# Kernel tuning notes

Measured on AMD Instinct MI355X. Metric: run time of the kernel, lower is better.

The kernel has to match this reference:

```python
import jax, jax.numpy as jnp
import numpy as np

B, S, D, H, SEP = 4, 2048, 768, 8, 102
Dh = D // H


def layer_norm(x, g, b, eps=1e-5):
    m = jnp.mean(x, axis=-1, keepdims=True)
    v = jnp.var(x, axis=-1, keepdims=True)
    return (x - m) / jnp.sqrt(v + eps) * g + b


def setup_inputs() -> dict:
    key = jax.random.key(0)
    ks = jax.random.split(key, 16)
    hidden_states = jax.random.normal(ks[0], (B, S, D), dtype=jnp.float32)
    # input_ids: random vocab ids avoiding SEP, with two SEP tokens planted per row
    rng = np.random.default_rng(0)
    ids = rng.integers(103, 30000, size=(B, S))
    for b in range(B):
        ids[b, S // 3 + 7 * b] = SEP
        ids[b, 2 * S // 3 + 11 * b] = SEP
    input_ids = jnp.asarray(ids, dtype=jnp.int64)
    attention_mask = jnp.ones((B, S), dtype=jnp.int32)
    sc = 0.02
    p = {}
    p['Wq'] = jax.random.normal(ks[1], (D, D), jnp.float32) * sc
    p['bq'] = jnp.zeros((D,), jnp.float32)
    p['Wk'] = jax.random.normal(ks[2], (D, D), jnp.float32) * sc
    p['bk'] = jnp.zeros((D,), jnp.float32)
    p['Wv'] = jax.random.normal(ks[3], (D, D), jnp.float32) * sc
    p['bv'] = jnp.zeros((D,), jnp.float32)
    p['Wo'] = jax.random.normal(ks[4], (D, D), jnp.float32) * sc
    p['bo'] = jnp.zeros((D,), jnp.float32)
    p['ln1_g'] = jnp.ones((D,), jnp.float32)
    p['ln1_b'] = jnp.zeros((D,), jnp.float32)
    p['W1'] = jax.random.normal(ks[5], (D, D), jnp.float32) * sc  # d_ff = d_model
    p['b1'] = jnp.zeros((D,), jnp.float32)
    p['W2'] = jax.random.normal(ks[6], (D, D), jnp.float32) * sc
    p['b2'] = jnp.zeros((D,), jnp.float32)
    p['ln2_g'] = jnp.ones((D,), jnp.float32)
    p['ln2_b'] = jnp.zeros((D,), jnp.float32)
    p['dn_g'] = jnp.ones((D,), jnp.float32)
    p['dn_b'] = jnp.zeros((D,), jnp.float32)
    return dict(hidden_states=hidden_states, input_ids=input_ids,
                attention_mask=attention_mask, **p)


def reference(hidden_states, input_ids, attention_mask,
              Wq, bq, Wk, bk, Wv, bv, Wo, bo, ln1_g, ln1_b,
              W1, b1, W2, b2, ln2_g, ln2_b, dn_g, dn_b):
    x = hidden_states
    # --- SEP-based ragged segment discovery (vectorized over batch) ---
    sep = input_ids == SEP                       # [B,S]
    idx = jnp.arange(S)
    big = S
    first = jnp.min(jnp.where(sep, idx, big), axis=-1)                       # [B]
    second = jnp.min(jnp.where(sep & (idx[None, :] > first[:, None]), idx, big), axis=-1)
    has2 = second < big                          # >= 2 SEP tokens present
    mid = S // 2
    src_end = jnp.where(has2, first, mid)
    hyp_start = jnp.where(has2, first + 1, mid)
    hyp_end = jnp.where(has2, second, S - 1)
    src_mask = (idx[None, :] >= 1) & (idx[None, :] < src_end[:, None])       # keys [B,S]
    hyp_mask = (idx[None, :] >= hyp_start[:, None]) & (idx[None, :] < hyp_end[:, None])
    valid = jnp.any(src_mask, -1) & jnp.any(hyp_mask, -1)                    # [B]

    # --- cross-attention: queries = hyp tokens, keys/values = src tokens ---
    q = (x @ Wq + bq).reshape(B, S, H, Dh)
    k = (x @ Wk + bk).reshape(B, S, H, Dh)
    v = (x @ Wv + bv).reshape(B, S, H, Dh)
    scores = jnp.einsum('bqhd,bkhd->bhqk', q, k) / jnp.sqrt(jnp.float32(Dh))
    scores = jnp.where(src_mask[:, None, None, :], scores, jnp.float32(-1e9))
    attn = jax.nn.softmax(scores, axis=-1)
    ctx = jnp.einsum('bhqk,bkhd->bqhd', attn, v).reshape(B, S, D)
    mha = ctx @ Wo + bo
    x1 = layer_norm(x + mha, ln1_g, ln1_b)
    ffn = jax.nn.gelu(x1 @ W1 + b1) @ W2 + b2
    x2 = layer_norm(x1 + ffn, ln2_g, ln2_b)      # updated_hyp

    # --- diff + LayerNorm, scatter back into hyp segment only ---
    diff = layer_norm(x2 - x, dn_g, dn_b)
    upd = hyp_mask & valid[:, None]
    return jnp.where(upd[..., None], x + diff, x)
```

## Files before the change

kernel.cpp:

```cpp
#include <hip/hip_runtime.h>
#include <math.h>

#define BB 4
#define SS 2048
#define DD 768
#define HH 8
#define DHD 96
#define SEP_ID 102
#define CHUNK 256
#define NCH_MAX 3
#define QT64 11
#define SLOTB 12800

typedef __attribute__((ext_vector_type(8))) short bf16x8;
typedef __attribute__((ext_vector_type(4))) float f32x4;

static __device__ __forceinline__ float gelu_tanh(float x) {
  float x3 = x * x * x;
  float t = tanhf(0.7978845608028654f * (x + 0.044715f * x3));
  return 0.5f * x * (1.0f + t);
}

static __device__ __forceinline__ unsigned short f2bf(float f) {
  unsigned int u = __float_as_uint(f);
  u = (u + 0x7FFF + ((u >> 16) & 1)) >> 16;
  return (unsigned short)u;
}

static __device__ __forceinline__ float bf2f(unsigned short u) {
  return __uint_as_float(((unsigned int)u) << 16);
}

#define MFMA16(A, B, C) __builtin_amdgcn_mfma_f32_16x16x32_bf16(A, B, C, 0, 0, 0)

static __device__ __forceinline__ void gl16(const void* g, void* l) {
  __builtin_amdgcn_global_load_lds(
      (__attribute__((address_space(1))) unsigned int*)g,
      (__attribute__((address_space(3))) unsigned int*)l, 16, 0, 0);
}

__global__ __launch_bounds__(256) void prep(
    const int* __restrict__ ids, int* __restrict__ seg,
    const float* __restrict__ x, unsigned short* __restrict__ xbf, int n4,
    const float* __restrict__ W0, const float* __restrict__ W1,
    const float* __restrict__ W2, const float* __restrict__ W3,
    const float* __restrict__ W4, const float* __restrict__ W5,
    unsigned short* __restrict__ Wt) {
  __shared__ char smem[64 * 65 * 4];
  int bx = blockIdx.x;
  if (bx < 4) {
    int* s1 = (int*)smem;
    int* s2 = s1 + 256;
    int b = bx;
    const int* row = ids + (size_t)b * SS;
    int m1 = SS, m2 = SS;
    for (int i = threadIdx.x; i < SS; i += 256) {
      if (row[i] == SEP_ID) {
        if (i < m1) { m2 = m1; m1 = i; }
        else if (i < m2) { m2 = i; }
      }
    }
    s1[threadIdx.x] = m1; s2[threadIdx.x] = m2;
    __syncthreads();
    for (int off = 128; off > 0; off >>= 1) {
      if (threadIdx.x < off) {
        int a1 = s1[threadIdx.x], a2 = s2[threadIdx.x];
        int b1 = s1[threadIdx.x + off], b2 = s2[threadIdx.x + off];
        s1[threadIdx.x] = min(a1, b1);
        s2[threadIdx.x] = min(max(a1, b1), min(a2, b2));
      }
      __syncthreads();
    }
    if (threadIdx.x == 0) {
      int first = s1[0], second = s2[0];
      bool has2 = (second < SS);
      int mid = SS / 2;
      int src_end = has2 ? first : mid;
      int hyp_lo = has2 ? (first + 1) : mid;
      int hyp_hi = has2 ? second : (SS - 1);
      int valid = ((src_end - 1) > 0 && (hyp_hi - hyp_lo) > 0) ? 1 : 0;
      if (!valid) { src_end = 1; hyp_lo = 0; hyp_hi = 0; }
      seg[b * 4 + 0] = src_end;
      seg[b * 4 + 1] = hyp_lo;
      seg[b * 4 + 2] = hyp_hi;
      seg[b * 4 + 3] = valid;
    }
  } else if (bx < 1540) {
    int i = (bx - 4) * 256 + threadIdx.x;
    int stride = 1536 * 256;
    const float4* xi = (const float4*)x;
    for (; i < n4; i += stride) {
      float4 v = xi[i];
      ushort4 r;
      r.x = f2bf(v.x); r.y = f2bf(v.y); r.z = f2bf(v.z); r.w = f2bf(v.w);
      *(ushort4*)(xbf + (size_t)i * 4) = r;
    }
  } else {
    float (*t)[65] = (float(*)[65])smem;
    int idx = bx - 1540;
    int z = idx / 144, rem = idx - z * 144;
    const float* W = (z == 0) ? W0 : (z == 1) ? W1 : (z == 2) ? W2
                    : (z == 3) ? W3 : (z == 4) ? W4 : W5;
    unsigned short* O = Wt + (size_t)z * DD * DD;
    int k0 = (rem / 12) * 64, n0 = (rem % 12) * 64;
    for (int i = threadIdx.x; i < 4096; i += 256) {
      int kk = i >> 6, nn = i & 63;
      t[kk][nn] = W[(size_t)(k0 + kk) * DD + n0 + nn];
    }
    __syncthreads();
    for (int i = threadIdx.x; i < 4096; i += 256) {
      int nn = i >> 6, kk = i & 63;
      O[(size_t)(n0 + nn) * DD + k0 + kk] = f2bf(t[kk][nn]);
    }
  }
}

__device__ __forceinline__ void gemm_core(
    const unsigned short* __restrict__ A, const unsigned short* __restrict__ Wt,
    const float* __restrict__ bias, unsigned short* __restrict__ C,
    int b, int row0, int hi, int col0, int which, float rs,
    unsigned short (*Al)[64 * 64], unsigned short (*Bl)[128 * 64]) {
  int tid = threadIdx.x, w = tid >> 6, lane = tid & 63;
  int llo = lane & 15, lhi = lane >> 4;
  int wrg = w >> 1, wcg = w & 1;

  const unsigned short* Ab = A + (size_t)b * SS * DD;

  f32x4 acc[2][4];
#pragma unroll
  for (int i = 0; i < 2; ++i)
#pragma unroll
    for (int j = 0; j < 4; ++j) acc[i][j] = (f32x4){0.f, 0.f, 0.f, 0.f};

  auto STAGE = [&](int t, int buf) {
    int kk = t * 64;
#pragma unroll
    for (int j = 0; j < 2; ++j) {
      int s = j * 256 + tid;
      int row = s >> 3, c = s & 7;
      int gr = min(row0 + row, hi - 1);
      gl16(Ab + (size_t)gr * DD + kk + ((c ^ (row & 7)) * 8),
           &Al[buf][(size_t)(j * 256 + w * 64) * 8]);
    }
#pragma unroll
    for (int j = 0; j < 4; ++j) {
      int s = j * 256 + tid;
      int row = s >> 3, c = s & 7;
      gl16(Wt + (size_t)(col0 + row) * DD + kk + ((c ^ (row & 7)) * 8),
           &Bl[buf][(size_t)(j * 256 + w * 64) * 8]);
    }
  };

  STAGE(0, 0);
  __syncthreads();
  for (int t = 0; t < DD / 64; ++t) {
    int cur = t & 1;
    if (t + 1 < DD / 64) STAGE(t + 1, cur ^ 1);
#pragma unroll
    for (int ksub = 0; ksub < 2; ++ksub) {
      bf16x8 af[2], bfr[4];
#pragma unroll
      for (int mi = 0; mi < 2; ++mi) {
        int lr = wrg * 32 + mi * 16 + llo;
        int slot = lr * 8 + ((ksub * 4 + lhi) ^ (lr & 7));
        af[mi] = *(const bf16x8*)&Al[cur][(size_t)slot * 8];
      }
#pragma unroll
      for (int ni = 0; ni < 4; ++ni) {
        int lr = wcg * 64 + ni * 16 + llo;
        int slot = lr * 8 + ((ksub * 4 + lhi) ^ (lr & 7));
        bfr[ni] = *(const bf16x8*)&Bl[cur][(size_t)slot * 8];
      }
#pragma unroll
      for (int mi = 0; mi < 2; ++mi)
#pragma unroll
        for (int ni = 0; ni < 4; ++ni)
          acc[mi][ni] = MFMA16(af[mi], bfr[ni], acc[mi][ni]);
    }
    __syncthreads();
  }

  float osc = (which == 0) ? rs : 1.f;
#pragma unroll
  for (int mi = 0; mi < 2; ++mi)
#pragma unroll
    for (int ni = 0; ni < 4; ++ni) {
      int col = col0 + wcg * 64 + ni * 16 + llo;
      float bsv = bias[col];
      int rowb = row0 + wrg * 32 + mi * 16 + lhi * 4;
#pragma unroll
      for (int r = 0; r < 4; ++r) {
        int row = rowb + r;
        if (which == 2) {
          float v = acc[mi][ni][r] + bsv;
          C[((size_t)b * DD + col) * SS + row] =
              (row < hi) ? f2bf(v) : (unsigned short)0;
        } else if (row < hi) {
          float v = (acc[mi][ni][r] + bsv) * osc;
          if (which == 4) v = gelu_tanh(v);
          C[((size_t)(b * SS + row)) * DD + col] = f2bf(v);
        }
      }
    }
}

__global__ __launch_bounds__(256) void gemm_qkv(
    const unsigned short* __restrict__ A, const unsigned short* __restrict__ Wt3,
    const float* __restrict__ bq, const float* __restrict__ bk, const float* __restrict__ bv,
    unsigned short* __restrict__ Qo, unsigned short* __restrict__ Ko,
    unsigned short* __restrict__ Vto, const int* __restrict__ seg, float rs) {
  __shared__ unsigned short Al[2][64 * 64];
  __shared__ unsigned short Bl[2][128 * 64];
  int b = blockIdx.z;
  int which = blockIdx.x / 6;
  int col0 = (blockIdx.x % 6) * 128;
  int lo = (which == 0) ? seg[b * 4 + 1] : 1;
  int hi = (which == 0) ? seg[b * 4 + 2] : seg[b * 4 + 0];
  int row0 = lo + (int)blockIdx.y * 64;
  if (row0 >= hi && !(which == 2 && row0 < hi + 64)) return;
  const unsigned short* Wt = Wt3 + (size_t)which * DD * DD;
  const float* bias = (which == 0) ? bq : (which == 1) ? bk : bv;
  unsigned short* C = (which == 0) ? Qo : (which == 1) ? Ko : Vto;
  gemm_core(A, Wt, bias, C, b, row0, hi, col0, which, rs, Al, Bl);
}

__global__ __launch_bounds__(256) void gemm_mfma(
    const unsigned short* __restrict__ A, const unsigned short* __restrict__ Wt,
    const float* __restrict__ bias, unsigned short* __restrict__ C,
    const int* __restrict__ seg, int gelu) {
  __shared__ unsigned short Al[2][64 * 64];
  __shared__ unsigned short Bl[2][128 * 64];
  int b = blockIdx.z;
  int lo = seg[b * 4 + 1], hi = seg[b * 4 + 2];
  int row0 = lo + (int)blockIdx.y * 64;
  if (row0 >= hi) return;
  gemm_core(A, Wt, bias, C, b, row0, hi, (int)blockIdx.x * 128,
            gelu ? 4 : 3, 1.f, Al, Bl);
}

__global__ __launch_bounds__(256) void attn_split(
    const unsigned short* __restrict__ Q, const unsigned short* __restrict__ K,
    const unsigned short* __restrict__ Vt, char* __restrict__ part,
    const int* __restrict__ seg) {
  int bh = blockIdx.z;
  int b = bh >> 3, h = bh & 7;
  int src_hi = seg[b * 4 + 0];
  int hyp_lo = seg[b * 4 + 1], hyp_hi = seg[b * 4 + 2];
  int q0b = hyp_lo + (int)blockIdx.x * 64;
  if (q0b >= hyp_hi) return;
  int ks = 1 + (int)blockIdx.y * CHUNK;
  if (ks >= src_hi) return;
  int ke = min(ks + CHUNK, src_hi);

  __shared__ unsigned short kls[64 * 128];
  __shared__ unsigned short vls[96 * 64];
  __shared__ unsigned short plds[4][1024];

  int tid = threadIdx.x;
  int w = tid >> 6, lane = tid & 63;
  int llo = lane & 15, lhi = lane >> 4;

  int qrow = min(q0b + w * 16 + llo, hyp_hi - 1);
  const unsigned short* qbase = Q + ((size_t)(b * SS + qrow)) * DD + h * DHD;
  bf16x8 qf[3];
#pragma unroll
  for (int df = 0; df < 3; ++df)
    qf[df] = *(const bf16x8*)(qbase + df * 32 + lhi * 8);

  const unsigned short* Kb = K + (size_t)b * SS * DD + h * DHD;
  const unsigned short* Vb = Vt + ((size_t)b * DD + h * DHD) * SS;

  f32x4 acc[6];
#pragma unroll
  for (int dt = 0; dt < 6; ++dt) acc[dt] = (f32x4){0.f, 0.f, 0.f, 0.f};
  float m_r[4] = {-1e30f, -1e30f, -1e30f, -1e30f};
  float l_r[4] = {0.f, 0.f, 0.f, 0.f};

  for (int k0 = ks; k0 < ke; k0 += 64) {
    __syncthreads();
#pragma unroll
    for (int p = 0; p < 3; ++p) {
      int idx = tid + p * 256;
      int row = idx / 12, slot = idx - row * 12;
      int krow = min(k0 + row, ke - 1);
      bf16x8 v = *(const bf16x8*)(Kb + (size_t)krow * DD + slot * 8);
      *(bf16x8*)&kls[row * 128 + ((slot ^ (row & 7)) << 3)] = v;
    }
#pragma unroll
    for (int p = 0; p < 3; ++p) {
      int idx = tid + p * 256;
      int row = idx >> 3, slot = idx & 7;
      bf16x8 v = *(const bf16x8*)(Vb + (size_t)row * SS + k0 + slot * 8);
      *(bf16x8*)&vls[row * 64 + ((slot ^ (row & 7)) << 3)] = v;
    }
    __syncthreads();
    f32x4 s[4];
#pragma unroll
    for (int t = 0; t < 4; ++t) {
      f32x4 st = (f32x4){0.f, 0.f, 0.f, 0.f};
      int row = t * 16 + llo;
#pragma unroll
      for (int df = 0; df < 3; ++df) {
        int slot = df * 4 + lhi;
        bf16x8 kf = *(const bf16x8*)&kls[row * 128 + ((slot ^ (row & 7)) << 3)];
        st = MFMA16(qf[df], kf, st);
      }
      s[t] = st;
    }
    float mx[4] = {-1e30f, -1e30f, -1e30f, -1e30f};
#pragma unroll
    for (int t = 0; t < 4; ++t) {
      bool kv = (k0 + t * 16 + llo) < ke;
#pragma unroll
      for (int r = 0; r < 4; ++r) {
        float sv = kv ? s[t][r] : -1e30f;
        s[t][r] = sv;
        mx[r] = fmaxf(mx[r], sv);
      }
    }
#pragma unroll
    for (int st = 1; st < 16; st <<= 1)
#pragma unroll
      for (int r = 0; r < 4; ++r) mx[r] = fmaxf(mx[r], __shfl_xor(mx[r], st));

    float p[4][4];
#pragma unroll
    for (int r = 0; r < 4; ++r) {
      float mn = fmaxf(m_r[r], mx[r]);
      float sc = __expf(m_r[r] - mn);
      m_r[r] = mn;
      l_r[r] *= sc;
#pragma unroll
      for (int dt = 0; dt < 6; ++dt) acc[dt][r] *= sc;
      float ps = 0.f;
#pragma unroll
      for (int t = 0; t < 4; ++t) {
        float pv = (s[t][r] > -1e29f) ? __expf(s[t][r] - mn) : 0.f;
        p[t][r] = pv;
        ps += pv;
      }
#pragma unroll
      for (int st = 1; st < 16; st <<= 1) ps += __shfl_xor(ps, st);
      l_r[r] += ps;
    }
#pragma unroll
    for (int t = 0; t < 4; ++t)
#pragma unroll
      for (int r = 0; r < 4; ++r) {
        int qq = lhi * 4 + r, kk = t * 16 + llo;
        plds[w][qq * 64 + (kk ^ ((qq & 7) << 3))] = f2bf(p[t][r]);
      }
    bf16x8 pa[2];
#pragma unroll
    for (int kh = 0; kh < 2; ++kh) {
      int idx = llo * 64 + ((lhi * 8 + kh * 32) ^ ((llo & 7) << 3));
      pa[kh] = *(const bf16x8*)&plds[w][idx];
    }
#pragma unroll
    for (int dt = 0; dt < 6; ++dt) {
      int row = dt * 16 + llo;
#pragma unroll
      for (int kh = 0; kh < 2; ++kh) {
        int slot = kh * 4 + lhi;
        bf16x8 vf = *(const bf16x8*)&vls[row * 64 + ((slot ^ (row & 7)) << 3)];
        acc[dt] = MFMA16(pa[kh], vf, acc[dt]);
      }
    }
  }
  char* slot = part + (((size_t)bh * QT64 + blockIdx.x) * NCH_MAX + blockIdx.y) * SLOTB;
  unsigned short* pacc = (unsigned short*)slot;
  float* pml = (float*)(slot + 12288);
#pragma unroll
  for (int r = 0; r < 4; ++r) {
    int qq = w * 16 + lhi * 4 + r;
#pragma unroll
    for (int dt = 0; dt < 6; ++dt)
      pacc[qq * 96 + dt * 16 + llo] = f2bf(acc[dt][r]);
    if (llo == 0) { pml[qq] = m_r[r]; pml[64 + qq] = l_r[r]; }
  }
}

__global__ __launch_bounds__(128) void attn_reduce(
    const char* __restrict__ part, unsigned short* __restrict__ ctx,
    const int* __restrict__ seg) {
  int bh = blockIdx.y;
  int b = bh >> 3, h = bh & 7;
  int src_hi = seg[b * 4 + 0];
  int hyp_lo = seg[b * 4 + 1], hyp_hi = seg[b * 4 + 2];
  int q0 = hyp_lo + (int)blockIdx.x * 16;
  if (q0 >= hyp_hi) return;
  int nch = (src_hi - 1 + CHUNK - 1) / CHUNK;
  if (nch > NCH_MAX) nch = NCH_MAX;
  int sub = blockIdx.x & 3;

  __shared__ float ml[NCH_MAX][32];
  __shared__ float Mg[16], invL[16], sc[NCH_MAX][16];
  int tid = threadIdx.x;
  const char* base = part + ((size_t)bh * QT64 + (blockIdx.x >> 2)) * NCH_MAX * SLOTB;
  for (int i = tid; i < 32 * nch; i += 128) {
    int c = i >> 5, j = i & 31;
    const float* pml = (const float*)(base + c * SLOTB + 12288);
    ml[c][j] = (j < 16) ? pml[sub * 16 + j] : pml[64 + sub * 16 + (j - 16)];
  }
  __syncthreads();
  if (tid < 16) {
    float mg = -1e30f;
    for (int c = 0; c < nch; ++c) mg = fmaxf(mg, ml[c][tid]);
    float lg = 0.f;
    for (int c = 0; c < nch; ++c) lg += ml[c][16 + tid] * __expf(ml[c][tid] - mg);
    Mg[tid] = mg;
    invL[tid] = 1.f / lg;
  }
  __syncthreads();
  for (int i = tid; i < 16 * nch; i += 128) {
    int c = i >> 4, q = i & 15;
    sc[c][q] = __expf(ml[c][q] - Mg[q]);
  }
  __syncthreads();
  for (int i = tid; i < 1536; i += 128) {
    int q = i / 96, d = i - q * 96;
    float v = 0.f;
    for (int c = 0; c < nch; ++c)
      v += bf2f(((const unsigned short*)(base + c * SLOTB))[(sub * 16 + q) * 96 + d]) * sc[c][q];
    int qq = q0 + q;
    if (qq < hyp_hi)
      ctx[((size_t)(b * SS + qq)) * DD + h * DHD + d] = f2bf(v * invL[q]);
  }
}

__device__ __forceinline__ float block_sum(float v, float* sbuf) {
#pragma unroll
  for (int off = 32; off > 0; off >>= 1) v += __shfl_xor(v, off);
  int lane = threadIdx.x & 63, w = threadIdx.x >> 6;
  __syncthreads();
  if (lane == 0) sbuf[w] = v;
  __syncthreads();
  return sbuf[0] + sbuf[1] + sbuf[2] + sbuf[3];
}

__global__ __launch_bounds__(256) void ln_residual(
    const float* __restrict__ X, const unsigned short* __restrict__ Yin,
    const float* __restrict__ g, const float* __restrict__ bta,
    float* __restrict__ Out, unsigned short* __restrict__ OutBf,
    const int* __restrict__ seg) {
  int b = blockIdx.y;
  int row = seg[b * 4 + 1] + (int)blockIdx.x;
  if (row >= seg[b * 4 + 2]) return;
  __shared__ float sbuf[4];
  size_t base = ((size_t)(b * SS + row)) * DD;
  int tid = threadIdx.x;
  float v[3];
  float sum = 0.f;
#pragma unroll
  for (int r = 0; r < 3; ++r) {
    int i = tid + r * 256;
    v[r] = X[base + i] + bf2f(Yin[base + i]);
    sum += v[r];
  }
  float mean = block_sum(sum, sbuf) * (1.f / DD);
  float vs = 0.f;
#pragma unroll
  for (int r = 0; r < 3; ++r) { float d = v[r] - mean; vs += d * d; }
  float var = block_sum(vs, sbuf) * (1.f / DD);
  float inv = rsqrtf(var + 1e-5f);
#pragma unroll
  for (int r = 0; r < 3; ++r) {
    int i = tid + r * 256;
    float o = (v[r] - mean) * inv * g[i] + bta[i];
    Out[base + i] = o;
    OutBf[base + i] = f2bf(o);
  }
}

__global__ __launch_bounds__(256) void ln2_diff_scatter(
    const float* __restrict__ X, const float* __restrict__ X1,
    const unsigned short* __restrict__ T2,
    const float* __restrict__ g2, const float* __restrict__ b2,
    const float* __restrict__ gd, const float* __restrict__ bd,
    float* __restrict__ Out, const int* __restrict__ seg) {
  int b = blockIdx.y, row = blockIdx.x;
  size_t base = ((size_t)(b * SS + row)) * DD;
  int tid = threadIdx.x;
  if (row < seg[b * 4 + 1] || row >= seg[b * 4 + 2]) {
#pragma unroll
    for (int r = 0; r < 3; ++r) {
      int i = tid + r * 256;
      Out[base + i] = X[base + i];
    }
    return;
  }
  __shared__ float sbuf[4];
  float y[3], xv[3];
  float sum = 0.f;
#pragma unroll
  for (int r = 0; r < 3; ++r) {
    int i = tid + r * 256;
    y[r] = X1[base + i] + bf2f(T2[base + i]);
    xv[r] = X[base + i];
    sum += y[r];
  }
  float mean = block_sum(sum, sbuf) * (1.f / DD);
  float vs = 0.f;
#pragma unroll
  for (int r = 0; r < 3; ++r) { float d = y[r] - mean; vs += d * d; }
  float var = block_sum(vs, sbuf) * (1.f / DD);
  float inv = rsqrtf(var + 1e-5f);
  float z[3];
  float sum2 = 0.f;
#pragma unroll
  for (int r = 0; r < 3; ++r) {
    int i = tid + r * 256;
    float x2 = (y[r] - mean) * inv * g2[i] + b2[i];
    z[r] = x2 - xv[r];
    sum2 += z[r];
  }
  float mean2 = block_sum(sum2, sbuf) * (1.f / DD);
  float vs2 = 0.f;
#pragma unroll
  for (int r = 0; r < 3; ++r) { float d = z[r] - mean2; vs2 += d * d; }
  float var2 = block_sum(vs2, sbuf) * (1.f / DD);
  float inv2 = rsqrtf(var2 + 1e-5f);
#pragma unroll
  for (int r = 0; r < 3; ++r) {
    int i = tid + r * 256;
    Out[base + i] = xv[r] + (z[r] - mean2) * inv2 * gd[i] + bd[i];
  }
}

extern "C" void kernel_launch(void* const* d_in, const int* in_sizes, int n_in,
                              void* d_out, int out_size, void* d_ws, size_t ws_size,
                              hipStream_t stream) {
  const float* x = (const float*)d_in[0];
  const int* ids = (const int*)d_in[1];
  const float* Wq = (const float*)d_in[3];
  const float* bq = (const float*)d_in[4];
  const float* Wk = (const float*)d_in[5];
  const float* bk = (const float*)d_in[6];
  const float* Wv = (const float*)d_in[7];
  const float* bv = (const float*)d_in[8];
  const float* Wo = (const float*)d_in[9];
  const float* bo = (const float*)d_in[10];
  const float* ln1g = (const float*)d_in[11];
  const float* ln1b = (const float*)d_in[12];
  const float* W1 = (const float*)d_in[13];
  const float* b1 = (const float*)d_in[14];
  const float* W2 = (const float*)d_in[15];
  const float* b2 = (const float*)d_in[16];
  const float* ln2g = (const float*)d_in[17];
  const float* ln2b = (const float*)d_in[18];
  const float* dng = (const float*)d_in[19];
  const float* dnb = (const float*)d_in[20];
  float* out = (float*)d_out;

  char* ws = (char*)d_ws;
  int* seg = (int*)ws;
  size_t NBH = (size_t)BB * SS * DD * 2;
  char* Ap = ws + 256;
  char* Bp = Ap + NBH;
  char* Cp = Bp + NBH;
  char* Dp = Cp + NBH;
  char* Fp = Dp + NBH + 8192;
  char* Gp = Fp + (size_t)BB * SS * DD * 4;

  unsigned short* x_bf = (unsigned short*)Ap;
  unsigned short* ctx_bf = (unsigned short*)Ap;
  unsigned short* h1_bf = (unsigned short*)Ap;
  unsigned short* q_bf = (unsigned short*)Bp;
  unsigned short* mha_bf = (unsigned short*)Bp;
  unsigned short* k_bf = (unsigned short*)Cp;
  unsigned short* t2_bf = (unsigned short*)Cp;
  unsigned short* vt_bf = (unsigned short*)Dp;
  unsigned short* x1_bf = (unsigned short*)Dp;
  char* part = Fp;
  float* x1f = (float*)Fp;
  unsigned short* wt = (unsigned short*)Gp;
  const size_t WSZ = (size_t)DD * DD;

  const float rs = 0.1020620726159658f;

  prep<<<2404, 256, 0, stream>>>(ids, seg, x, x_bf, BB * SS * DD / 4,
                                 Wq, Wk, Wv, Wo, W1, W2, wt);

  gemm_qkv<<<dim3(18, 12, BB), 256, 0, stream>>>(
      x_bf, wt, bq, bk, bv, q_bf, k_bf, vt_bf, seg, rs);

  attn_split<<<dim3(QT64, NCH_MAX, 32), 256, 0, stream>>>(q_bf, k_bf, vt_bf, part, seg);
  attn_reduce<<<dim3(44, 32), 128, 0, stream>>>(part, ctx_bf, seg);

  gemm_mfma<<<dim3(6, 11, BB), 256, 0, stream>>>(ctx_bf, wt + 3 * WSZ, bo, mha_bf, seg, 0);
  ln_residual<<<dim3(704, BB), 256, 0, stream>>>(x, mha_bf, ln1g, ln1b, x1f, x1_bf, seg);
  gemm_mfma<<<dim3(6, 11, BB), 256, 0, stream>>>(x1_bf, wt + 4 * WSZ, b1, h1_bf, seg, 1);
  gemm_mfma<<<dim3(6, 11, BB), 256, 0, stream>>>(h1_bf, wt + 5 * WSZ, b2, t2_bf, seg, 0);
  ln2_diff_scatter<<<dim3(SS, BB), 256, 0, stream>>>(x, x1f, t2_bf, ln2g, ln2b, dng, dnb, out, seg);
}
```

Measured before the change: 166.3 us.

## Halve GEMM K-tile to 32, drop swizzle, and remove fp32 x1 buffer

The shared GEMM core now stages a K-depth of 32 instead of 64 per iteration, with one A load and two B loads per thread and no XOR swizzle on LDS addresses. This halves LDS use per block, which may raise occupancy, but it doubles the number of barrier-synchronised iterations and may bring back LDS bank conflicts. Separately, the first LayerNorm no longer writes an fp32 copy of x1; the final LN kernel reads the bf16 copy instead. That saves a global write and read but lowers the precision of the residual path.

```diff
diff --git a/kernel.cpp b/kernel.cpp
--- a/kernel.cpp
+++ b/kernel.cpp
@@ -119,7 +119,7 @@
     const unsigned short* __restrict__ A, const unsigned short* __restrict__ Wt,
     const float* __restrict__ bias, unsigned short* __restrict__ C,
     int b, int row0, int hi, int col0, int which, float rs,
-    unsigned short (*Al)[64 * 64], unsigned short (*Bl)[128 * 64]) {
+    unsigned short (*Al)[64 * 32], unsigned short (*Bl)[128 * 32]) {
   int tid = threadIdx.x, w = tid >> 6, lane = tid & 63;
   int llo = lane & 15, lhi = lane >> 4;
   int wrg = w >> 1, wcg = w & 1;
@@ -132,51 +132,43 @@
 #pragma unroll
     for (int j = 0; j < 4; ++j) acc[i][j] = (f32x4){0.f, 0.f, 0.f, 0.f};
 
+  int arow = tid >> 2, ac = tid & 3;
+  int agr = min(row0 + arow, hi - 1);
+  const unsigned short* asrc = Ab + (size_t)agr * DD + ac * 8;
+
   auto STAGE = [&](int t, int buf) {
-    int kk = t * 64;
+    int kk = t * 32;
+    gl16(asrc + kk, &Al[buf][(size_t)(w * 64) * 8]);
 #pragma unroll
     for (int j = 0; j < 2; ++j) {
       int s = j * 256 + tid;
-      int row = s >> 3, c = s & 7;
-      int gr = min(row0 + row, hi - 1);
-      gl16(Ab + (size_t)gr * DD + kk + ((c ^ (row & 7)) * 8),
-           &Al[buf][(size_t)(j * 256 + w * 64) * 8]);
-    }
-#pragma unroll
-    for (int j = 0; j < 4; ++j) {
-      int s = j * 256 + tid;
-      int row = s >> 3, c = s & 7;
-      gl16(Wt + (size_t)(col0 + row) * DD + kk + ((c ^ (row & 7)) * 8),
+      int row = s >> 2, c = s & 3;
+      gl16(Wt + (size_t)(col0 + row) * DD + kk + c * 8,
            &Bl[buf][(size_t)(j * 256 + w * 64) * 8]);
     }
   };
 
   STAGE(0, 0);
   __syncthreads();
-  for (int t = 0; t < DD / 64; ++t) {
+  for (int t = 0; t < DD / 32; ++t) {
     int cur = t & 1;
-    if (t + 1 < DD / 64) STAGE(t + 1, cur ^ 1);
-#pragma unroll
-    for (int ksub = 0; ksub < 2; ++ksub) {
-      bf16x8 af[2], bfr[4];
-#pragma unroll
-      for (int mi = 0; mi < 2; ++mi) {
-        int lr = wrg * 32 + mi * 16 + llo;
-        int slot = lr * 8 + ((ksub * 4 + lhi) ^ (lr & 7));
-        af[mi] = *(const bf16x8*)&Al[cur][(size_t)slot * 8];
-      }
-#pragma unroll
-      for (int ni = 0; ni < 4; ++ni) {
-        int lr = wcg * 64 + ni * 16 + llo;
-        int slot = lr * 8 + ((ksub * 4 + lhi) ^ (lr & 7));
-        bfr[ni] = *(const bf16x8*)&Bl[cur][(size_t)slot * 8];
-      }
-#pragma unroll
-      for (int mi = 0; mi < 2; ++mi)
-#pragma unroll
-        for (int ni = 0; ni < 4; ++ni)
-          acc[mi][ni] = MFMA16(af[mi], bfr[ni], acc[mi][ni]);
-    }
+    if (t + 1 < DD / 32) STAGE(t + 1, cur ^ 1);
+    bf16x8 af[2], bfr[4];
+#pragma unroll
+    for (int mi = 0; mi < 2; ++mi) {
+      int lr = wrg * 32 + mi * 16 + llo;
+      af[mi] = *(const bf16x8*)&Al[cur][lr * 32 + lhi * 8];
+    }
+#pragma unroll
+    for (int ni = 0; ni < 4; ++ni) {
+      int lr = wcg * 64 + ni * 16 + llo;
+      bfr[ni] = *(const bf16x8*)&Bl[cur][lr * 32 + lhi * 8];
+    }
+#pragma unroll
+    for (int mi = 0; mi < 2; ++mi)
+#pragma unroll
+      for (int ni = 0; ni < 4; ++ni)
+        acc[mi][ni] = MFMA16(af[mi], bfr[ni], acc[mi][ni]);
     __syncthreads();
   }
 
@@ -209,8 +201,8 @@
     const float* __restrict__ bq, const float* __restrict__ bk, const float* __restrict__ bv,
     unsigned short* __restrict__ Qo, unsigned short* __restrict__ Ko,
     unsigned short* __restrict__ Vto, const int* __restrict__ seg, float rs) {
-  __shared__ unsigned short Al[2][64 * 64];
-  __shared__ unsigned short Bl[2][128 * 64];
+  __shared__ unsigned short Al[2][64 * 32];
+  __shared__ unsigned short Bl[2][128 * 32];
   int b = blockIdx.z;
   int which = blockIdx.x / 6;
   int col0 = (blockIdx.x % 6) * 128;
@@ -228,8 +220,8 @@
     const unsigned short* __restrict__ A, const unsigned short* __restrict__ Wt,
     const float* __restrict__ bias, unsigned short* __restrict__ C,
     const int* __restrict__ seg, int gelu) {
-  __shared__ unsigned short Al[2][64 * 64];
-  __shared__ unsigned short Bl[2][128 * 64];
+  __shared__ unsigned short Al[2][64 * 32];
+  __shared__ unsigned short Bl[2][128 * 32];
   int b = blockIdx.z;
   int lo = seg[b * 4 + 1], hi = seg[b * 4 + 2];
   int row0 = lo + (int)blockIdx.y * 64;
@@ -441,8 +433,7 @@
 __global__ __launch_bounds__(256) void ln_residual(
     const float* __restrict__ X, const unsigned short* __restrict__ Yin,
     const float* __restrict__ g, const float* __restrict__ bta,
-    float* __restrict__ Out, unsigned short* __restrict__ OutBf,
-    const int* __restrict__ seg) {
+    unsigned short* __restrict__ OutBf, const int* __restrict__ seg) {
   int b = blockIdx.y;
   int row = seg[b * 4 + 1] + (int)blockIdx.x;
   if (row >= seg[b * 4 + 2]) return;
@@ -466,14 +457,12 @@
 #pragma unroll
   for (int r = 0; r < 3; ++r) {
     int i = tid + r * 256;
-    float o = (v[r] - mean) * inv * g[i] + bta[i];
-    Out[base + i] = o;
-    OutBf[base + i] = f2bf(o);
+    OutBf[base + i] = f2bf((v[r] - mean) * inv * g[i] + bta[i]);
   }
 }
 
 __global__ __launch_bounds__(256) void ln2_diff_scatter(
-    const float* __restrict__ X, const float* __restrict__ X1,
+    const float* __restrict__ X, const unsigned short* __restrict__ X1,
     const unsigned short* __restrict__ T2,
     const float* __restrict__ g2, const float* __restrict__ b2,
     const float* __restrict__ gd, const float* __restrict__ bd,
@@ -495,7 +484,7 @@
 #pragma unroll
   for (int r = 0; r < 3; ++r) {
     int i = tid + r * 256;
-    y[r] = X1[base + i] + bf2f(T2[base + i]);
+    y[r] = bf2f(X1[base + i]) + bf2f(T2[base + i]);
     xv[r] = X[base + i];
     sum += y[r];
   }
@@ -572,7 +561,6 @@
   unsigned short* vt_bf = (unsigned short*)Dp;
   unsigned short* x1_bf = (unsigned short*)Dp;
   char* part = Fp;
-  float* x1f = (float*)Fp;
   unsigned short* wt = (unsigned short*)Gp;
   const size_t WSZ = (size_t)DD * DD;
 
@@ -588,8 +576,8 @@
   attn_reduce<<<dim3(44, 32), 128, 0, stream>>>(part, ctx_bf, seg);
 
   gemm_mfma<<<dim3(6, 11, BB), 256, 0, stream>>>(ctx_bf, wt + 3 * WSZ, bo, mha_bf, seg, 0);
-  ln_residual<<<dim3(704, BB), 256, 0, stream>>>(x, mha_bf, ln1g, ln1b, x1f, x1_bf, seg);
+  ln_residual<<<dim3(704, BB), 256, 0, stream>>>(x, mha_bf, ln1g, ln1b, x1_bf, seg);
   gemm_mfma<<<dim3(6, 11, BB), 256, 0, stream>>>(x1_bf, wt + 4 * WSZ, b1, h1_bf, seg, 1);
   gemm_mfma<<<dim3(6, 11, BB), 256, 0, stream>>>(h1_bf, wt + 5 * WSZ, b2, t2_bf, seg, 0);
-  ln2_diff_scatter<<<dim3(SS, BB), 256, 0, stream>>>(x, x1f, t2_bf, ln2g, ln2b, dng, dnb, out, seg);
-}
+  ln2_diff_scatter<<<dim3(SS, BB), 256, 0, stream>>>(x, x1_bf, t2_bf, ln2g, ln2b, dng, dnb, out, seg);
+}
```

Result: no change. 168.4 us (+1.2%).
